# Kernel optimization log

Measured on AMD Instinct MI355X. Metric: run time of the kernel, lower is better.

## Reference

```python
import jax, jax.numpy as jnp
import numpy as np

H, W = 256, 256
N = 512


def setup_inputs() -> dict:
    key = jax.random.key(0)
    k1, k2, k3, k4, k5 = jax.random.split(key, 5)
    # gaussian centers in front of the camera
    xy = jax.random.normal(k1, (N, 2), dtype=jnp.float32) * 3.0
    z = jax.random.uniform(k2, (N,), dtype=jnp.float32, minval=2.0, maxval=45.0)
    means3D = jnp.concatenate([xy, z[:, None]], axis=1)  # (N,3)
    # SPD 3x3 covariances
    A = jax.random.normal(k3, (N, 3, 3), dtype=jnp.float32) * 0.2
    covs3d = jnp.einsum('nij,nkj->nik', A, A) + 0.05 * jnp.eye(3, dtype=jnp.float32)
    colors = jax.random.uniform(k4, (N, 3), dtype=jnp.float32)
    opacities = jax.random.uniform(k5, (N,), dtype=jnp.float32)
    K = jnp.array([[300.0, 0.0, W / 2.0], [0.0, 300.0, H / 2.0], [0.0, 0.0, 1.0]], dtype=jnp.float32)
    R = jnp.eye(3, dtype=jnp.float32)
    t = jnp.zeros((3,), dtype=jnp.float32)
    return {"means3D": means3D, "covs3d": covs3d, "colors": colors,
            "opacities": opacities, "K": K, "R": R, "t": t}


def _render(means3D, covs3d, colors, opacities, K, R, t):
    # --- projection ---
    cam = means3D @ R.T + t                       # (N,3)
    Z = cam[:, 2]                                 # raw camera-space depth
    depths = jnp.maximum(Z, 1.0)                  # clamped (used for sort/mask)
    screen = cam @ K.T
    means2D = screen[:, :2] / screen[:, 2:3]      # (N,2)
    fx, fy = K[0, 0], K[1, 1]
    zeros = jnp.zeros_like(Z)
    # Jacobian of perspective projection, (N,2,3); uses raw Z as in the original
    J = jnp.stack([
        jnp.stack([fx / Z, zeros, -fx * cam[:, 0] / (Z * Z)], axis=-1),
        jnp.stack([zeros, fy / Z, -fy * cam[:, 1] / (Z * Z)], axis=-1),
    ], axis=1)
    covs_cam = jnp.einsum('ij,njk,lk->nil', R, covs3d, R)     # R Sigma R^T
    covs2D = jnp.einsum('nij,njk,nlk->nil', J, covs_cam, J)   # J Sigma_cam J^T, (N,2,2)

    valid = (depths > 1.0) & (depths < 50.0)
    # front-to-back sort by clamped depth
    idx = jnp.argsort(depths)
    means2D = means2D[idx]
    covs2D = covs2D[idx]
    colors_s = colors[idx]
    op_s = opacities[idx]
    valid = valid[idx]

    # --- per-gaussian per-pixel density ---
    covs2D = covs2D + 1e-4 * jnp.eye(2, dtype=covs2D.dtype)
    cov_inv = jnp.linalg.inv(covs2D)              # (N,2,2)
    cov_det = jnp.linalg.det(covs2D)              # (N,)
    norm = 1.0 / (2.0 * jnp.pi * jnp.sqrt(cov_det))

    ys, xs = jnp.meshgrid(jnp.arange(H, dtype=jnp.float32),
                          jnp.arange(W, dtype=jnp.float32), indexing='ij')
    pixels = jnp.stack([xs, ys], axis=-1)         # (H,W,2), [x,y]

    dx = pixels[None] - means2D[:, None, None, :]                 # (N,H,W,2)
    expo = -0.5 * jnp.einsum('nhwi,nij,nhwj->nhw', dx, cov_inv, dx)
    gaussian = norm[:, None, None] * jnp.exp(expo)                # (N,H,W)
    gaussian = gaussian * valid.astype(gaussian.dtype)[:, None, None]

    # --- alpha compositing (inclusive cumprod as in the original) ---
    alphas = op_s[:, None, None] * gaussian                       # (N,H,W)
    T = jnp.cumprod(1.0 - alphas, axis=0)
    weights = alphas * T
    rendered = jnp.einsum('nhw,nc->hwc', weights, colors_s)       # (H,W,3)
    return rendered


def reference(means3D, covs3d, colors, opacities, K, R, t):
    return _render(means3D, covs3d, colors, opacities, K, R, t)
```

## Files before the change

### kernel.cpp

```cpp
#include <hip/hip_runtime.h>


constexpr int   REC   = 16;
constexpr int   WIMG  = 256;
constexpr int   HIMG  = 256;
constexpr int   SPLIT = 8;
constexpr float LOG2E  = 1.4426950408889634f;
constexpr float INV2PI = 0.15915494309189535f;
constexpr float INVEPS = 1.0e7f;

__global__ __launch_bounds__(512) void gs_preprocess(
    const float* __restrict__ means3D, const float* __restrict__ covs3d,
    const float* __restrict__ colors,  const float* __restrict__ opac,
    const float* __restrict__ Km,      const float* __restrict__ Rm,
    const float* __restrict__ tvec,    float* __restrict__ recs, int N)
{
    __shared__ float s_depth[512];
    __shared__ int   s_cnt[64][9];
    const int t  = threadIdx.x;
    const int l  = t & 63, p = t >> 6;
    const int gi = (int)blockIdx.x * 64 + l;

    float d_all = 3.0e38f;
    if (t < N) {
        const float m0 = means3D[t*3+0], m1 = means3D[t*3+1], m2 = means3D[t*3+2];
        d_all = fmaxf(Rm[6]*m0 + Rm[7]*m1 + Rm[8]*m2 + tvec[2], 1.0f);
    }
    s_depth[t] = d_all;
    __syncthreads();

    const float dg = s_depth[gi & 511];
    int cnt = 0;
    #pragma unroll 16
    for (int j = p*64; j < p*64 + 64; ++j) {
        const float dj = s_depth[j];
        cnt += (dj < dg) || (dj == dg && j < gi);
    }
    s_cnt[l][p] = cnt;

    float rec[13];
    const bool act = (p == 0) && (gi < N);
    if (act) {
        float Kl[9], Rl[9], tl[3];
        #pragma unroll
        for (int k = 0; k < 9; ++k) { Kl[k] = Km[k]; Rl[k] = Rm[k]; }
        tl[0] = tvec[0]; tl[1] = tvec[1]; tl[2] = tvec[2];

        const float m0 = means3D[gi*3+0], m1 = means3D[gi*3+1], m2 = means3D[gi*3+2];
        const float cam0 = Rl[0]*m0 + Rl[1]*m1 + Rl[2]*m2 + tl[0];
        const float cam1 = Rl[3]*m0 + Rl[4]*m1 + Rl[5]*m2 + tl[1];
        const float cam2 = Rl[6]*m0 + Rl[7]*m1 + Rl[8]*m2 + tl[2];
        const float Z = cam2;
        const float depth = fmaxf(Z, 1.0f);

        const float s0 = Kl[0]*cam0 + Kl[1]*cam1 + Kl[2]*cam2;
        const float s1 = Kl[3]*cam0 + Kl[4]*cam1 + Kl[5]*cam2;
        const float s2 = Kl[6]*cam0 + Kl[7]*cam1 + Kl[8]*cam2;
        const float mx = s0 / s2, my = s1 / s2;

        const float fx = Kl[0], fy = Kl[4];
        const float iz = 1.0f / Z;
        float J[2][3];
        J[0][0] = fx*iz; J[0][1] = 0.0f;  J[0][2] = -fx*cam0*iz*iz;
        J[1][0] = 0.0f;  J[1][1] = fy*iz; J[1][2] = -fy*cam1*iz*iz;

        float S[9];
        #pragma unroll
        for (int k = 0; k < 9; ++k) S[k] = covs3d[gi*9+k];

        float RS[9], Cc[9];
        #pragma unroll
        for (int r = 0; r < 3; ++r)
            #pragma unroll
            for (int c = 0; c < 3; ++c)
                RS[r*3+c] = Rl[r*3+0]*S[0+c] + Rl[r*3+1]*S[3+c] + Rl[r*3+2]*S[6+c];
        #pragma unroll
        for (int r = 0; r < 3; ++r)
            #pragma unroll
            for (int c = 0; c < 3; ++c)
                Cc[r*3+c] = RS[r*3+0]*Rl[c*3+0] + RS[r*3+1]*Rl[c*3+1] + RS[r*3+2]*Rl[c*3+2];

        float JC[2][3];
        #pragma unroll
        for (int r = 0; r < 2; ++r)
            #pragma unroll
            for (int c = 0; c < 3; ++c)
                JC[r][c] = J[r][0]*Cc[0+c] + J[r][1]*Cc[3+c] + J[r][2]*Cc[6+c];

        const float c200 = JC[0][0]*J[0][0] + JC[0][1]*J[0][1] + JC[0][2]*J[0][2] + 1e-4f;
        const float c201 = JC[0][0]*J[1][0] + JC[0][1]*J[1][1] + JC[0][2]*J[1][2];
        const float c210 = JC[1][0]*J[0][0] + JC[1][1]*J[0][1] + JC[1][2]*J[0][2];
        const float c211 = JC[1][0]*J[1][0] + JC[1][1]*J[1][1] + JC[1][2]*J[1][2] + 1e-4f;

        const float det  = c200*c211 - c201*c210;
        const float idet = 1.0f / det;
        const float ia   = c211*idet;
        const float i01  = -0.5f*(c201 + c210)*idet;
        const float ic   = c200*idet;
        const float ibs  = 2.0f*i01;

        const bool  valid = (depth > 1.0f) && (depth < 50.0f);
        const float nrm   = valid ? (INV2PI / sqrtf(det)) : 0.0f;
        const float opn   = opac[gi] * nrm;

        const float c1 = i01 / ia;
        const float c2 = ic - i01*i01/ia;
        const float L2 = 2.0f * logf(opn * INVEPS);

        rec[0]  = my;  rec[1] = c2;  rec[2] = L2;  rec[3] = c1;
        rec[4]  = mx;  rec[5] = ia;
        rec[6]  = -0.5f*LOG2E*ia;
        rec[7]  = -0.5f*LOG2E*ibs;
        rec[8]  = -0.5f*LOG2E*ic;
        rec[9]  = opn;
        rec[10] = colors[gi*3+0];
        rec[11] = colors[gi*3+1];
        rec[12] = colors[gi*3+2];
    }
    __syncthreads();

    if (act) {
        int rank = 0;
        #pragma unroll
        for (int q = 0; q < 8; ++q) rank += s_cnt[l][q];
        float4* dst = (float4*)(recs + rank*REC);
        dst[0] = make_float4(rec[0],  rec[1],  rec[2],  rec[3]);
        dst[1] = make_float4(rec[4],  rec[5],  rec[6],  rec[7]);
        dst[2] = make_float4(rec[8],  rec[9],  rec[10], rec[11]);
        dst[3] = make_float4(rec[12], 0.0f,    0.0f,    0.0f);
    }
}

__global__ __launch_bounds__(512, 4) void gs_render(
    const float* __restrict__ recs, float* __restrict__ out, int N)
{
    __shared__ float  s_my[512], s_c2[512], s_L2[512], s_c1[512], s_mx[512], s_p0[512];
    __shared__ float  s_ev[512][12];
    __shared__ int    s_hits[SPLIT][64];
    __shared__ float4 s_part[2][SPLIT][64];
    __shared__ float  s_rgb[2][192];

    const int t = threadIdx.x;

    if (t < N) {
        const float4 a = *(const float4*)(recs + t*REC + 0);
        const float4 b = *(const float4*)(recs + t*REC + 4);
        const float4 c = *(const float4*)(recs + t*REC + 8);
        const float4 d = *(const float4*)(recs + t*REC + 12);
        s_my[t] = a.x; s_c2[t] = a.y; s_L2[t] = a.z; s_c1[t] = a.w;
        s_mx[t] = b.x; s_p0[t] = b.y;
        float4* ev = (float4*)s_ev[t];
        ev[0] = make_float4(b.x, a.x, b.z, b.w);
        ev[1] = make_float4(c.x, c.y, c.z, c.w);
        s_ev[t][8] = d.x;
    } else {
        s_my[t] = 0.0f; s_c2[t] = 0.0f; s_L2[t] = -1e30f;
        s_c1[t] = 0.0f; s_mx[t] = 0.0f; s_p0[t] = 1.0f;
    }
    __syncthreads();

    const int w    = t >> 6;
    const int lane = t & 63;
    const int xs   = (int)blockIdx.x & 3;
    const int pr   = (int)blockIdx.x >> 2;
    const float y0f = (float)(2*pr);
    const float sx0 = (float)(xs * 64);
    const float scx = sx0 + 31.5f;
    const float px  = sx0 + (float)lane;

    const int base = w * 64;
    bool hit;
    {
        const int j = base + lane;
        const float myj = s_my[j], c2 = s_c2[j], L2 = s_L2[j];
        const float c1  = s_c1[j], mxj = s_mx[j], p0 = s_p0[j];
        float dy  = y0f - myj;
        float rem = fmaf(-c2, dy*dy, L2);
        float xc  = fmaf(-c1, dy, mxj);
        float t1  = fmaxf(fabsf(xc - scx) - 31.5f, 0.0f);
        const bool h0 = (p0*t1*t1 <= rem);
        dy  = dy + 1.0f;
        rem = fmaf(-c2, dy*dy, L2);
        xc  = xc - c1;
        t1  = fmaxf(fabsf(xc - scx) - 31.5f, 0.0f);
        const bool h1 = (p0*t1*t1 <= rem);
        hit = h0 | h1;
    }
    const unsigned long long mask = __ballot(hit);
    const int nhit = __popcll(mask);
    if (hit) {
        const int pos = __popcll(mask & ((1ull << lane) - 1ull));
        s_hits[w][pos] = base + lane;
    }

    float T0 = 1.0f, r0 = 0.0f, g0 = 0.0f, b0 = 0.0f;
    float T1 = 1.0f, r1 = 0.0f, g1 = 0.0f, b1 = 0.0f;

    for (int i = 0; i < nhit; ++i) {
        const int j = s_hits[w][i];
        const float* e = s_ev[j];
        const float4 v0 = *(const float4*)(e + 0);
        const float4 v1 = *(const float4*)(e + 4);
        const float  bl = e[8];

        const float dx   = px - v0.x;
        const float adx2 = v0.z * dx * dx;
        const float u    = v0.w * dx;
        const float dy0  = y0f - v0.y;
        const float dy1  = dy0 + 1.0f;
        const float e20  = fmaf(dy0, fmaf(v1.x, dy0, u), adx2);
        const float e21  = fmaf(dy1, fmaf(v1.x, dy1, u), adx2);
        const float al0  = v1.y * __builtin_amdgcn_exp2f(e20);
        const float al1  = v1.y * __builtin_amdgcn_exp2f(e21);

        T0 *= (1.0f - al0);
        const float w0 = al0 * T0;
        r0 = fmaf(w0, v1.z, r0); g0 = fmaf(w0, v1.w, g0); b0 = fmaf(w0, bl, b0);

        T1 *= (1.0f - al1);
        const float w1 = al1 * T1;
        r1 = fmaf(w1, v1.z, r1); g1 = fmaf(w1, v1.w, g1); b1 = fmaf(w1, bl, b1);
    }

    s_part[0][w][lane] = make_float4(T0, r0, g0, b0);
    s_part[1][w][lane] = make_float4(T1, r1, g1, b1);
    __syncthreads();

    if (t < 128) {
        const int row = t >> 6, p = t & 63;
        float4 f = s_part[row][0][p];
        float Ta = f.x, r_ = f.y, g_ = f.z, b_ = f.w;
        #pragma unroll
        for (int k = 1; k < SPLIT; ++k) {
            const float4 q = s_part[row][k][p];
            r_ = fmaf(Ta, q.y, r_);
            g_ = fmaf(Ta, q.z, g_);
            b_ = fmaf(Ta, q.w, b_);
            Ta *= q.x;
        }
        s_rgb[row][p*3+0] = r_;
        s_rgb[row][p*3+1] = g_;
        s_rgb[row][p*3+2] = b_;
    }
    __syncthreads();

    if (t < 384) {
        const int row = t / 192, i = t - row * 192;
        out[(2*pr + row) * (WIMG*3) + xs*192 + i] = s_rgb[row][i];
    }
}

extern "C" void kernel_launch(void* const* d_in, const int* in_sizes, int n_in,
                              void* d_out, int out_size, void* d_ws, size_t ws_size,
                              hipStream_t stream)
{
    const float* means3D = (const float*)d_in[0];
    const float* covs3d  = (const float*)d_in[1];
    const float* colors  = (const float*)d_in[2];
    const float* opac    = (const float*)d_in[3];
    const float* Km      = (const float*)d_in[4];
    const float* Rm      = (const float*)d_in[5];
    const float* tv      = (const float*)d_in[6];
    const int N = in_sizes[3];

    float* recs = (float*)d_ws;
    float* out  = (float*)d_out;

    gs_preprocess<<<dim3((N + 63) / 64), dim3(512), 0, stream>>>(
        means3D, covs3d, colors, opac, Km, Rm, tv, recs, N);

    gs_render<<<dim3(WIMG * HIMG / 128), dim3(512), 0, stream>>>(recs, out, N);
}
```

Measured before the change: 15.78 us.

## Fuse preprocessing and depth sort into render kernel, recomputing per block

Merges the preprocess and render kernels into one. Each of the 512 render blocks now projects all gaussians, ranks them by depth with a full 512-element shared-memory scan per thread, and scatters the records straight into shared memory. This removes a kernel launch, the workspace round trip and the dependency between the two launches. In exchange every block repeats the preprocessing and the O(N) rank count, which adds redundant global loads and ALU work per block and raises register pressure under the 4-blocks launch bound.

```diff
diff --git a/kernel.cpp b/kernel.cpp
--- a/kernel.cpp
+++ b/kernel.cpp
@@ -1,7 +1,6 @@
 #include <hip/hip_runtime.h>
 
 
-constexpr int   REC   = 16;
 constexpr int   WIMG  = 256;
 constexpr int   HIMG  = 256;
 constexpr int   SPLIT = 8;
@@ -9,17 +8,20 @@
 constexpr float INV2PI = 0.15915494309189535f;
 constexpr float INVEPS = 1.0e7f;
 
-__global__ __launch_bounds__(512) void gs_preprocess(
+__global__ __launch_bounds__(512, 4) void gs_fused(
     const float* __restrict__ means3D, const float* __restrict__ covs3d,
     const float* __restrict__ colors,  const float* __restrict__ opac,
     const float* __restrict__ Km,      const float* __restrict__ Rm,
-    const float* __restrict__ tvec,    float* __restrict__ recs, int N)
+    const float* __restrict__ tvec,    float* __restrict__ out, int N)
 {
-    __shared__ float s_depth[512];
-    __shared__ int   s_cnt[64][9];
-    const int t  = threadIdx.x;
-    const int l  = t & 63, p = t >> 6;
-    const int gi = (int)blockIdx.x * 64 + l;
+    __shared__ float  s_depth[512];
+    __shared__ float  s_my[512], s_c2[512], s_L2[512], s_c1[512], s_mx[512], s_p0[512];
+    __shared__ float  s_ev[512][12];
+    __shared__ int    s_hits[SPLIT][64];
+    __shared__ float4 s_part[2][SPLIT][64];
+    __shared__ float  s_rgb[2][192];
+
+    const int t = threadIdx.x;
 
     float d_all = 3.0e38f;
     if (t < N) {
@@ -27,26 +29,19 @@
         d_all = fmaxf(Rm[6]*m0 + Rm[7]*m1 + Rm[8]*m2 + tvec[2], 1.0f);
     }
     s_depth[t] = d_all;
-    __syncthreads();
-
-    const float dg = s_depth[gi & 511];
-    int cnt = 0;
-    #pragma unroll 16
-    for (int j = p*64; j < p*64 + 64; ++j) {
-        const float dj = s_depth[j];
-        cnt += (dj < dg) || (dj == dg && j < gi);
-    }
-    s_cnt[l][p] = cnt;
+    s_my[t] = 0.0f; s_c2[t] = 0.0f; s_L2[t] = -1e30f;
+    s_c1[t] = 0.0f; s_mx[t] = 0.0f; s_p0[t] = 1.0f;
+    __syncthreads();
 
     float rec[13];
-    const bool act = (p == 0) && (gi < N);
+    const bool act = (t < N);
     if (act) {
         float Kl[9], Rl[9], tl[3];
         #pragma unroll
         for (int k = 0; k < 9; ++k) { Kl[k] = Km[k]; Rl[k] = Rm[k]; }
         tl[0] = tvec[0]; tl[1] = tvec[1]; tl[2] = tvec[2];
 
-        const float m0 = means3D[gi*3+0], m1 = means3D[gi*3+1], m2 = means3D[gi*3+2];
+        const float m0 = means3D[t*3+0], m1 = means3D[t*3+1], m2 = means3D[t*3+2];
         const float cam0 = Rl[0]*m0 + Rl[1]*m1 + Rl[2]*m2 + tl[0];
         const float cam1 = Rl[3]*m0 + Rl[4]*m1 + Rl[5]*m2 + tl[1];
         const float cam2 = Rl[6]*m0 + Rl[7]*m1 + Rl[8]*m2 + tl[2];
@@ -66,7 +61,7 @@
 
         float S[9];
         #pragma unroll
-        for (int k = 0; k < 9; ++k) S[k] = covs3d[gi*9+k];
+        for (int k = 0; k < 9; ++k) S[k] = covs3d[t*9+k];
 
         float RS[9], Cc[9];
         #pragma unroll
@@ -101,7 +96,7 @@
 
         const bool  valid = (depth > 1.0f) && (depth < 50.0f);
         const float nrm   = valid ? (INV2PI / sqrtf(det)) : 0.0f;
-        const float opn   = opac[gi] * nrm;
+        const float opn   = opac[t] * nrm;
 
         const float c1 = i01 / ia;
         const float c2 = ic - i01*i01/ia;
@@ -113,49 +108,33 @@
         rec[7]  = -0.5f*LOG2E*ibs;
         rec[8]  = -0.5f*LOG2E*ic;
         rec[9]  = opn;
-        rec[10] = colors[gi*3+0];
-        rec[11] = colors[gi*3+1];
-        rec[12] = colors[gi*3+2];
-    }
-    __syncthreads();
+        rec[10] = colors[t*3+0];
+        rec[11] = colors[t*3+1];
+        rec[12] = colors[t*3+2];
+    }
+
+    int rank = 0;
+    {
+        const float dg = d_all;
+        const float4* d4 = (const float4*)s_depth;
+        #pragma unroll 4
+        for (int j4 = 0; j4 < 128; ++j4) {
+            const float4 v = d4[j4];
+            const int j = 4*j4;
+            rank += (v.x < dg) || (v.x == dg && (j+0) < t);
+            rank += (v.y < dg) || (v.y == dg && (j+1) < t);
+            rank += (v.z < dg) || (v.z == dg && (j+2) < t);
+            rank += (v.w < dg) || (v.w == dg && (j+3) < t);
+        }
+    }
 
     if (act) {
-        int rank = 0;
-        #pragma unroll
-        for (int q = 0; q < 8; ++q) rank += s_cnt[l][q];
-        float4* dst = (float4*)(recs + rank*REC);
-        dst[0] = make_float4(rec[0],  rec[1],  rec[2],  rec[3]);
-        dst[1] = make_float4(rec[4],  rec[5],  rec[6],  rec[7]);
-        dst[2] = make_float4(rec[8],  rec[9],  rec[10], rec[11]);
-        dst[3] = make_float4(rec[12], 0.0f,    0.0f,    0.0f);
-    }
-}
-
-__global__ __launch_bounds__(512, 4) void gs_render(
-    const float* __restrict__ recs, float* __restrict__ out, int N)
-{
-    __shared__ float  s_my[512], s_c2[512], s_L2[512], s_c1[512], s_mx[512], s_p0[512];
-    __shared__ float  s_ev[512][12];
-    __shared__ int    s_hits[SPLIT][64];
-    __shared__ float4 s_part[2][SPLIT][64];
-    __shared__ float  s_rgb[2][192];
-
-    const int t = threadIdx.x;
-
-    if (t < N) {
-        const float4 a = *(const float4*)(recs + t*REC + 0);
-        const float4 b = *(const float4*)(recs + t*REC + 4);
-        const float4 c = *(const float4*)(recs + t*REC + 8);
-        const float4 d = *(const float4*)(recs + t*REC + 12);
-        s_my[t] = a.x; s_c2[t] = a.y; s_L2[t] = a.z; s_c1[t] = a.w;
-        s_mx[t] = b.x; s_p0[t] = b.y;
-        float4* ev = (float4*)s_ev[t];
-        ev[0] = make_float4(b.x, a.x, b.z, b.w);
-        ev[1] = make_float4(c.x, c.y, c.z, c.w);
-        s_ev[t][8] = d.x;
-    } else {
-        s_my[t] = 0.0f; s_c2[t] = 0.0f; s_L2[t] = -1e30f;
-        s_c1[t] = 0.0f; s_mx[t] = 0.0f; s_p0[t] = 1.0f;
+        s_my[rank] = rec[0]; s_c2[rank] = rec[1]; s_L2[rank] = rec[2];
+        s_c1[rank] = rec[3]; s_mx[rank] = rec[4]; s_p0[rank] = rec[5];
+        float4* ev = (float4*)s_ev[rank];
+        ev[0] = make_float4(rec[4], rec[0], rec[6], rec[7]);
+        ev[1] = make_float4(rec[8], rec[9], rec[10], rec[11]);
+        s_ev[rank][8] = rec[12];
     }
     __syncthreads();
 
@@ -263,11 +242,8 @@
     const float* tv      = (const float*)d_in[6];
     const int N = in_sizes[3];
 
-    float* recs = (float*)d_ws;
-    float* out  = (float*)d_out;
-
-    gs_preprocess<<<dim3((N + 63) / 64), dim3(512), 0, stream>>>(
-        means3D, covs3d, colors, opac, Km, Rm, tv, recs, N);
-
-    gs_render<<<dim3(WIMG * HIMG / 128), dim3(512), 0, stream>>>(recs, out, N);
+    float* out = (float*)d_out;
+
+    gs_fused<<<dim3(WIMG * HIMG / 128), dim3(512), 0, stream>>>(
+        means3D, covs3d, colors, opac, Km, Rm, tv, out, N);
 }
```

Result: slower. 36.41 us (+130.7%).

## Fuse preprocess and render into one kernel with atomic flag barrier

Applied to the files above, without the earlier changes.

Merges the preprocessing and rendering kernels into one launch. The first few blocks compute the sorted gaussian records, then signal completion through a global atomic counter, and every block spin-waits on that counter before rendering. The aim is to remove the second kernel launch and the gap between kernels. In exchange it adds a memset launch, spin-wait latency, and a deadlock risk if the producer blocks are not scheduled before the waiting blocks.

```diff
diff --git a/kernel.cpp b/kernel.cpp
--- a/kernel.cpp
+++ b/kernel.cpp
@@ -9,138 +9,150 @@
 constexpr float INV2PI = 0.15915494309189535f;
 constexpr float INVEPS = 1.0e7f;
 
-__global__ __launch_bounds__(512) void gs_preprocess(
+__global__ __launch_bounds__(512, 4) void gs_fused(
     const float* __restrict__ means3D, const float* __restrict__ covs3d,
     const float* __restrict__ colors,  const float* __restrict__ opac,
     const float* __restrict__ Km,      const float* __restrict__ Rm,
-    const float* __restrict__ tvec,    float* __restrict__ recs, int N)
+    const float* __restrict__ tvec,    float* __restrict__ recs,
+    unsigned int* __restrict__ flag,   float* __restrict__ out, int N)
 {
     __shared__ float s_depth[512];
     __shared__ int   s_cnt[64][9];
-    const int t  = threadIdx.x;
-    const int l  = t & 63, p = t >> 6;
-    const int gi = (int)blockIdx.x * 64 + l;
-
-    float d_all = 3.0e38f;
-    if (t < N) {
-        const float m0 = means3D[t*3+0], m1 = means3D[t*3+1], m2 = means3D[t*3+2];
-        d_all = fmaxf(Rm[6]*m0 + Rm[7]*m1 + Rm[8]*m2 + tvec[2], 1.0f);
-    }
-    s_depth[t] = d_all;
-    __syncthreads();
-
-    const float dg = s_depth[gi & 511];
-    int cnt = 0;
-    #pragma unroll 16
-    for (int j = p*64; j < p*64 + 64; ++j) {
-        const float dj = s_depth[j];
-        cnt += (dj < dg) || (dj == dg && j < gi);
-    }
-    s_cnt[l][p] = cnt;
-
-    float rec[13];
-    const bool act = (p == 0) && (gi < N);
-    if (act) {
-        float Kl[9], Rl[9], tl[3];
-        #pragma unroll
-        for (int k = 0; k < 9; ++k) { Kl[k] = Km[k]; Rl[k] = Rm[k]; }
-        tl[0] = tvec[0]; tl[1] = tvec[1]; tl[2] = tvec[2];
-
-        const float m0 = means3D[gi*3+0], m1 = means3D[gi*3+1], m2 = means3D[gi*3+2];
-        const float cam0 = Rl[0]*m0 + Rl[1]*m1 + Rl[2]*m2 + tl[0];
-        const float cam1 = Rl[3]*m0 + Rl[4]*m1 + Rl[5]*m2 + tl[1];
-        const float cam2 = Rl[6]*m0 + Rl[7]*m1 + Rl[8]*m2 + tl[2];
-        const float Z = cam2;
-        const float depth = fmaxf(Z, 1.0f);
-
-        const float s0 = Kl[0]*cam0 + Kl[1]*cam1 + Kl[2]*cam2;
-        const float s1 = Kl[3]*cam0 + Kl[4]*cam1 + Kl[5]*cam2;
-        const float s2 = Kl[6]*cam0 + Kl[7]*cam1 + Kl[8]*cam2;
-        const float mx = s0 / s2, my = s1 / s2;
-
-        const float fx = Kl[0], fy = Kl[4];
-        const float iz = 1.0f / Z;
-        float J[2][3];
-        J[0][0] = fx*iz; J[0][1] = 0.0f;  J[0][2] = -fx*cam0*iz*iz;
-        J[1][0] = 0.0f;  J[1][1] = fy*iz; J[1][2] = -fy*cam1*iz*iz;
-
-        float S[9];
-        #pragma unroll
-        for (int k = 0; k < 9; ++k) S[k] = covs3d[gi*9+k];
-
-        float RS[9], Cc[9];
-        #pragma unroll
-        for (int r = 0; r < 3; ++r)
-            #pragma unroll
-            for (int c = 0; c < 3; ++c)
-                RS[r*3+c] = Rl[r*3+0]*S[0+c] + Rl[r*3+1]*S[3+c] + Rl[r*3+2]*S[6+c];
-        #pragma unroll
-        for (int r = 0; r < 3; ++r)
-            #pragma unroll
-            for (int c = 0; c < 3; ++c)
-                Cc[r*3+c] = RS[r*3+0]*Rl[c*3+0] + RS[r*3+1]*Rl[c*3+1] + RS[r*3+2]*Rl[c*3+2];
-
-        float JC[2][3];
-        #pragma unroll
-        for (int r = 0; r < 2; ++r)
-            #pragma unroll
-            for (int c = 0; c < 3; ++c)
-                JC[r][c] = J[r][0]*Cc[0+c] + J[r][1]*Cc[3+c] + J[r][2]*Cc[6+c];
-
-        const float c200 = JC[0][0]*J[0][0] + JC[0][1]*J[0][1] + JC[0][2]*J[0][2] + 1e-4f;
-        const float c201 = JC[0][0]*J[1][0] + JC[0][1]*J[1][1] + JC[0][2]*J[1][2];
-        const float c210 = JC[1][0]*J[0][0] + JC[1][1]*J[0][1] + JC[1][2]*J[0][2];
-        const float c211 = JC[1][0]*J[1][0] + JC[1][1]*J[1][1] + JC[1][2]*J[1][2] + 1e-4f;
-
-        const float det  = c200*c211 - c201*c210;
-        const float idet = 1.0f / det;
-        const float ia   = c211*idet;
-        const float i01  = -0.5f*(c201 + c210)*idet;
-        const float ic   = c200*idet;
-        const float ibs  = 2.0f*i01;
-
-        const bool  valid = (depth > 1.0f) && (depth < 50.0f);
-        const float nrm   = valid ? (INV2PI / sqrtf(det)) : 0.0f;
-        const float opn   = opac[gi] * nrm;
-
-        const float c1 = i01 / ia;
-        const float c2 = ic - i01*i01/ia;
-        const float L2 = 2.0f * logf(opn * INVEPS);
-
-        rec[0]  = my;  rec[1] = c2;  rec[2] = L2;  rec[3] = c1;
-        rec[4]  = mx;  rec[5] = ia;
-        rec[6]  = -0.5f*LOG2E*ia;
-        rec[7]  = -0.5f*LOG2E*ibs;
-        rec[8]  = -0.5f*LOG2E*ic;
-        rec[9]  = opn;
-        rec[10] = colors[gi*3+0];
-        rec[11] = colors[gi*3+1];
-        rec[12] = colors[gi*3+2];
-    }
-    __syncthreads();
-
-    if (act) {
-        int rank = 0;
-        #pragma unroll
-        for (int q = 0; q < 8; ++q) rank += s_cnt[l][q];
-        float4* dst = (float4*)(recs + rank*REC);
-        dst[0] = make_float4(rec[0],  rec[1],  rec[2],  rec[3]);
-        dst[1] = make_float4(rec[4],  rec[5],  rec[6],  rec[7]);
-        dst[2] = make_float4(rec[8],  rec[9],  rec[10], rec[11]);
-        dst[3] = make_float4(rec[12], 0.0f,    0.0f,    0.0f);
-    }
-}
-
-__global__ __launch_bounds__(512, 4) void gs_render(
-    const float* __restrict__ recs, float* __restrict__ out, int N)
-{
     __shared__ float  s_my[512], s_c2[512], s_L2[512], s_c1[512], s_mx[512], s_p0[512];
     __shared__ float  s_ev[512][12];
     __shared__ int    s_hits[SPLIT][64];
     __shared__ float4 s_part[2][SPLIT][64];
     __shared__ float  s_rgb[2][192];
 
-    const int t = threadIdx.x;
+    const int bid  = (int)blockIdx.x;
+    const int t    = threadIdx.x;
+    const int nPre = (N + 63) / 64;
+
+    if (bid < nPre) {
+        const int l  = t & 63, p = t >> 6;
+        const int gi = bid * 64 + l;
+
+        float d_all = 3.0e38f;
+        if (t < N) {
+            const float m0 = means3D[t*3+0], m1 = means3D[t*3+1], m2 = means3D[t*3+2];
+            d_all = fmaxf(Rm[6]*m0 + Rm[7]*m1 + Rm[8]*m2 + tvec[2], 1.0f);
+        }
+        s_depth[t] = d_all;
+        __syncthreads();
+
+        const float dg = s_depth[gi & 511];
+        int cnt = 0;
+        #pragma unroll 16
+        for (int j = p*64; j < p*64 + 64; ++j) {
+            const float dj = s_depth[j];
+            cnt += (dj < dg) || (dj == dg && j < gi);
+        }
+        s_cnt[l][p] = cnt;
+
+        float rec[13];
+        const bool act = (p == 0) && (gi < N);
+        if (act) {
+            float Kl[9], Rl[9], tl[3];
+            #pragma unroll
+            for (int k = 0; k < 9; ++k) { Kl[k] = Km[k]; Rl[k] = Rm[k]; }
+            tl[0] = tvec[0]; tl[1] = tvec[1]; tl[2] = tvec[2];
+
+            const float m0 = means3D[gi*3+0], m1 = means3D[gi*3+1], m2 = means3D[gi*3+2];
+            const float cam0 = Rl[0]*m0 + Rl[1]*m1 + Rl[2]*m2 + tl[0];
+            const float cam1 = Rl[3]*m0 + Rl[4]*m1 + Rl[5]*m2 + tl[1];
+            const float cam2 = Rl[6]*m0 + Rl[7]*m1 + Rl[8]*m2 + tl[2];
+            const float Z = cam2;
+            const float depth = fmaxf(Z, 1.0f);
+
+            const float s0 = Kl[0]*cam0 + Kl[1]*cam1 + Kl[2]*cam2;
+            const float s1 = Kl[3]*cam0 + Kl[4]*cam1 + Kl[5]*cam2;
+            const float s2 = Kl[6]*cam0 + Kl[7]*cam1 + Kl[8]*cam2;
+            const float mx = s0 / s2, my = s1 / s2;
+
+            const float fx = Kl[0], fy = Kl[4];
+            const float iz = 1.0f / Z;
+            float J[2][3];
+            J[0][0] = fx*iz; J[0][1] = 0.0f;  J[0][2] = -fx*cam0*iz*iz;
+            J[1][0] = 0.0f;  J[1][1] = fy*iz; J[1][2] = -fy*cam1*iz*iz;
+
+            float S[9];
+            #pragma unroll
+            for (int k = 0; k < 9; ++k) S[k] = covs3d[gi*9+k];
+
+            float RS[9], Cc[9];
+            #pragma unroll
+            for (int r = 0; r < 3; ++r)
+                #pragma unroll
+                for (int c = 0; c < 3; ++c)
+                    RS[r*3+c] = Rl[r*3+0]*S[0+c] + Rl[r*3+1]*S[3+c] + Rl[r*3+2]*S[6+c];
+            #pragma unroll
+            for (int r = 0; r < 3; ++r)
+                #pragma unroll
+                for (int c = 0; c < 3; ++c)
+                    Cc[r*3+c] = RS[r*3+0]*Rl[c*3+0] + RS[r*3+1]*Rl[c*3+1] + RS[r*3+2]*Rl[c*3+2];
+
+            float JC[2][3];
+            #pragma unroll
+            for (int r = 0; r < 2; ++r)
+                #pragma unroll
+                for (int c = 0; c < 3; ++c)
+                    JC[r][c] = J[r][0]*Cc[0+c] + J[r][1]*Cc[3+c] + J[r][2]*Cc[6+c];
+
+            const float c200 = JC[0][0]*J[0][0] + JC[0][1]*J[0][1] + JC[0][2]*J[0][2] + 1e-4f;
+            const float c201 = JC[0][0]*J[1][0] + JC[0][1]*J[1][1] + JC[0][2]*J[1][2];
+            const float c210 = JC[1][0]*J[0][0] + JC[1][1]*J[0][1] + JC[1][2]*J[0][2];
+            const float c211 = JC[1][0]*J[1][0] + JC[1][1]*J[1][1] + JC[1][2]*J[1][2] + 1e-4f;
+
+            const float det  = c200*c211 - c201*c210;
+            const float idet = 1.0f / det;
+            const float ia   = c211*idet;
+            const float i01  = -0.5f*(c201 + c210)*idet;
+            const float ic   = c200*idet;
+            const float ibs  = 2.0f*i01;
+
+            const bool  valid = (depth > 1.0f) && (depth < 50.0f);
+            const float nrm   = valid ? (INV2PI / sqrtf(det)) : 0.0f;
+            const float opn   = opac[gi] * nrm;
+
+            const float c1 = i01 / ia;
+            const float c2 = ic - i01*i01/ia;
+            const float L2 = 2.0f * logf(opn * INVEPS);
+
+            rec[0]  = my;  rec[1] = c2;  rec[2] = L2;  rec[3] = c1;
+            rec[4]  = mx;  rec[5] = ia;
+            rec[6]  = -0.5f*LOG2E*ia;
+            rec[7]  = -0.5f*LOG2E*ibs;
+            rec[8]  = -0.5f*LOG2E*ic;
+            rec[9]  = opn;
+            rec[10] = colors[gi*3+0];
+            rec[11] = colors[gi*3+1];
+            rec[12] = colors[gi*3+2];
+        }
+        __syncthreads();
+
+        if (act) {
+            int rank = 0;
+            #pragma unroll
+            for (int q = 0; q < 8; ++q) rank += s_cnt[l][q];
+            float4* dst = (float4*)(recs + rank*REC);
+            dst[0] = make_float4(rec[0],  rec[1],  rec[2],  rec[3]);
+            dst[1] = make_float4(rec[4],  rec[5],  rec[6],  rec[7]);
+            dst[2] = make_float4(rec[8],  rec[9],  rec[10], rec[11]);
+            dst[3] = make_float4(rec[12], 0.0f,    0.0f,    0.0f);
+        }
+        __syncthreads();
+
+        if (t == 0) {
+            __threadfence();
+            __hip_atomic_fetch_add(flag, 1u, __ATOMIC_RELEASE, __HIP_MEMORY_SCOPE_AGENT);
+        }
+    }
+
+    if (t == 0) {
+        while ((int)__hip_atomic_load(flag, __ATOMIC_ACQUIRE, __HIP_MEMORY_SCOPE_AGENT) < nPre)
+            __builtin_amdgcn_s_sleep(1);
+    }
+    __syncthreads();
 
     if (t < N) {
         const float4 a = *(const float4*)(recs + t*REC + 0);
@@ -161,8 +173,8 @@
 
     const int w    = t >> 6;
     const int lane = t & 63;
-    const int xs   = (int)blockIdx.x & 3;
-    const int pr   = (int)blockIdx.x >> 2;
+    const int xs   = bid & 3;
+    const int pr   = bid >> 2;
     const float y0f = (float)(2*pr);
     const float sx0 = (float)(xs * 64);
     const float scx = sx0 + 31.5f;
@@ -263,11 +275,12 @@
     const float* tv      = (const float*)d_in[6];
     const int N = in_sizes[3];
 
-    float* recs = (float*)d_ws;
-    float* out  = (float*)d_out;
-
-    gs_preprocess<<<dim3((N + 63) / 64), dim3(512), 0, stream>>>(
-        means3D, covs3d, colors, opac, Km, Rm, tv, recs, N);
-
-    gs_render<<<dim3(WIMG * HIMG / 128), dim3(512), 0, stream>>>(recs, out, N);
+    float*        recs = (float*)d_ws;
+    unsigned int* flag = (unsigned int*)((char*)d_ws + 64*1024);
+
+    hipMemsetAsync(flag, 0, sizeof(unsigned int), stream);
+
+    gs_fused<<<dim3(WIMG * HIMG / 128), dim3(512), 0, stream>>>(
+        means3D, covs3d, colors, opac, Km, Rm, tv,
+        recs, flag, (float*)d_out, N);
 }
```

Measured after the change: 38.33 us. +142.9%, slower.
